# Kernel optimization log

Hardware: AMD Instinct MI355X
Metric: run time of the kernel (lower is better)

The kernel has to match this reference:

```python
import jax, jax.numpy as jnp
import numpy as np
from jax import lax

B, HH, WW, C = 8, 128, 128, 192
FL = 3  # focal_level
HID = 4 * C

def _gelu(x):
    return jax.nn.gelu(x, approximate=False)

def _ln(x, g, b, eps=1e-5):
    m = jnp.mean(x, axis=-1, keepdims=True)
    v = jnp.mean(jnp.square(x - m), axis=-1, keepdims=True)
    return (x - m) * lax.rsqrt(v + eps) * g + b

def _dwconv(x, k):
    # x: (B,C,H,W), k: (C,kh,kw) depthwise kernel
    return lax.conv_general_dilated(x, k[:, None], (1, 1), 'SAME',
                                    feature_group_count=x.shape[1],
                                    dimension_numbers=('NCHW', 'OIHW', 'NCHW'))

def setup_inputs() -> dict:
    key = jax.random.key(0)
    ks = jax.random.split(key, 12)
    s = 0.02
    return {
        'x': jax.random.normal(ks[0], (B, HH * WW, C), jnp.float32),
        'ln1_g': jnp.ones((C,), jnp.float32),
        'ln1_b': jnp.zeros((C,), jnp.float32),
        'f_w': jax.random.normal(ks[1], (C, 2 * C + FL + 1), jnp.float32) * s,
        'f_b': jnp.zeros((2 * C + FL + 1,), jnp.float32),
        'fk0': jax.random.normal(ks[2], (C, 3, 3), jnp.float32) * s,
        'fk1': jax.random.normal(ks[3], (C, 5, 5), jnp.float32) * s,
        'fk2': jax.random.normal(ks[4], (C, 7, 7), jnp.float32) * s,
        'h_w': jax.random.normal(ks[5], (C, C), jnp.float32) * s,
        'h_b': jnp.zeros((C,), jnp.float32),
        'proj_w': jax.random.normal(ks[6], (C, C), jnp.float32) * s,
        'proj_b': jnp.zeros((C,), jnp.float32),
        'ln2_g': jnp.ones((C,), jnp.float32),
        'ln2_b': jnp.zeros((C,), jnp.float32),
        'fc1_w': jax.random.normal(ks[7], (C, HID), jnp.float32) * s,
        'fc1_b': jnp.zeros((HID,), jnp.float32),
        'fc2_w': jax.random.normal(ks[8], (HID, C), jnp.float32) * s,
        'fc2_b': jnp.zeros((C,), jnp.float32),
        'H': HH,
        'W': WW,
    }

def reference(x, ln1_g, ln1_b, f_w, f_b, fk0, fk1, fk2, h_w, h_b,
              proj_w, proj_b, ln2_g, ln2_b, fc1_w, fc1_b, fc2_w, fc2_b, H, W):
    b, L, c = x.shape
    shortcut = x
    t = _ln(x, ln1_g, ln1_b).reshape(b, H, W, c)
    # f projection: (B,H,W,2C+FL+1) -> (B, 2C+FL+1, H, W)
    f = (t @ f_w + f_b).transpose(0, 3, 1, 2)
    q, ctx, gates = f[:, :c], f[:, c:2 * c], f[:, 2 * c:]
    ctx_all = jnp.zeros_like(ctx)
    for l, k in enumerate((fk0, fk1, fk2)):
        ctx = _gelu(_dwconv(ctx, k))
        ctx_all = ctx_all + ctx * gates[:, l:l + 1]
    ctx_global = _gelu(jnp.mean(ctx, axis=(2, 3), keepdims=True))
    ctx_all = ctx_all + ctx_global * gates[:, FL:]
    # h: 1x1 conv over channels
    modulator = jnp.einsum('oc,bchw->bohw', h_w, ctx_all) + h_b[None, :, None, None]
    x_out = (q * modulator).transpose(0, 2, 3, 1)  # (B,H,W,C)
    x_out = (x_out @ proj_w + proj_b).reshape(b, L, c)
    x1 = shortcut + x_out
    y = _ln(x1, ln2_g, ln2_b)
    y = _gelu(y @ fc1_w + fc1_b) @ fc2_w + fc2_b
    return x1 + y
```

## Files before the change

### kernel.cpp

```cpp
#include <hip/hip_runtime.h>
#include <hip/hip_bf16.h>

#define BB   8
#define HGT  128
#define WID  128
#define CC   192
#define LLEN (HGT*WID)
#define MM   (BB*LLEN)
#define NF   388
#define HIDN 768

typedef unsigned short us16;
typedef __attribute__((ext_vector_type(8))) short bf16x8;
typedef __attribute__((ext_vector_type(4))) float f32x4;

__device__ __forceinline__ float bf2f(us16 u) {
    return __uint_as_float(((unsigned int)u) << 16);
}
__device__ __forceinline__ us16 f2bf(float f) {
    unsigned int x = __float_as_uint(f);
    x = (x + 0x7fffu + ((x >> 16) & 1u)) >> 16;
    return (us16)x;
}
__device__ __forceinline__ float gelu_f(float x) {
    float u = 0.7978845608f * x * (1.0f + 0.044715f * x * x);
    float e = __expf(fminf(2.0f * u, 30.0f));
    return 0.5f * x * (1.0f + (e - 1.0f) / (e + 1.0f));
}

__device__ __forceinline__ void gload_lds16(const void* g, void* l) {
    __builtin_amdgcn_global_load_lds(
        (const __attribute__((address_space(1))) void*)g,
        (__attribute__((address_space(3))) void*)l, 16, 0, 0);
}

__global__ __launch_bounds__(256) void wcvt_kernel(const float* __restrict__ f_w,
        const float* __restrict__ h_w, const float* __restrict__ proj_w,
        const float* __restrict__ fc1_w, const float* __restrict__ fc2_w,
        const float* __restrict__ fk0, const float* __restrict__ fk1,
        const float* __restrict__ fk2,
        us16* __restrict__ fwT, us16* __restrict__ hwB, us16* __restrict__ projT,
        us16* __restrict__ w1T, us16* __restrict__ w2T,
        us16* __restrict__ kw0T, us16* __restrict__ kw1T, us16* __restrict__ kw2T) {
    int i = blockIdx.x * 256 + threadIdx.x;
    if (i < 86016) {
        int n = i / 192, k = i % 192;
        fwT[i] = (n < NF) ? f2bf(f_w[k * NF + n]) : (us16)0;
        return;
    }
    i -= 86016;
    if (i < 36864) { hwB[i] = f2bf(h_w[i]); return; }
    i -= 36864;
    if (i < 36864) { int n = i / 192, k = i % 192; projT[i] = f2bf(proj_w[k * CC + n]); return; }
    i -= 36864;
    if (i < 147456) { int n = i / 192, k = i % 192; w1T[i] = f2bf(fc1_w[k * HIDN + n]); return; }
    i -= 147456;
    if (i < 147456) { int n = i / 768, k = i % 768; w2T[i] = f2bf(fc2_w[k * CC + n]); return; }
    i -= 147456;
    if (i < 1728)  { int kyx = i / 192, c = i % 192; kw0T[i] = f2bf(fk0[c * 9 + kyx]);  return; }
    i -= 1728;
    if (i < 4800)  { int kyx = i / 192, c = i % 192; kw1T[i] = f2bf(fk1[c * 25 + kyx]); return; }
    i -= 4800;
    if (i < 9408)  { int kyx = i / 192, c = i % 192; kw2T[i] = f2bf(fk2[c * 49 + kyx]); return; }
}

__global__ __launch_bounds__(256) void ln_kernel(const float* __restrict__ in,
                                                 const float* __restrict__ g,
                                                 const float* __restrict__ b,
                                                 us16* __restrict__ out) {
    int wid  = threadIdx.x >> 6;
    int lane = threadIdx.x & 63;
    int row  = blockIdx.x * 4 + wid;
    const float* p = in + (size_t)row * CC;
    float v0 = p[lane], v1 = p[lane + 64], v2 = p[lane + 128];
    float s1 = v0 + v1 + v2;
    float s2 = v0*v0 + v1*v1 + v2*v2;
    for (int o = 32; o; o >>= 1) { s1 += __shfl_xor(s1, o); s2 += __shfl_xor(s2, o); }
    float m   = s1 * (1.0f / 192.0f);
    float var = s2 * (1.0f / 192.0f) - m * m;
    float inv = rsqrtf(var + 1e-5f);
    us16* q = out + (size_t)row * CC;
    q[lane]       = f2bf((v0 - m) * inv * g[lane]       + b[lane]);
    q[lane + 64]  = f2bf((v1 - m) * inv * g[lane + 64]  + b[lane + 64]);
    q[lane + 128] = f2bf((v2 - m) * inv * g[lane + 128] + b[lane + 128]);
}

template<int MODE>
__global__ __launch_bounds__(256) void mgemm_kernel(const us16* __restrict__ A,
        const us16* __restrict__ Bt, const float* __restrict__ bias,
        us16* __restrict__ out_q, us16* __restrict__ out_ctx, us16* __restrict__ out_g,
        const us16* __restrict__ q_in, const us16* __restrict__ gates_in,
        const float* __restrict__ hg, const float* __restrict__ x_in,
        float* __restrict__ out_f) {
    __shared__ __align__(16) char Asm[128 * 384];
    constexpr int NT = (MODE == 0) ? 7 : 3;
    int id  = blockIdx.x;
    int xcd = id & 7;
    int s   = id >> 3;
    int mt  = xcd * 128 + s / NT;
    int nt  = s % NT;
    int m0 = mt * 128, n0 = nt * 64;
    int tid = threadIdx.x, lane = tid & 63, w = tid >> 6;
    int wm = w >> 1, wn = w & 1, g = lane >> 4, lr = lane & 15;

    const char* Agl = (const char*)(A + (size_t)m0 * CC);
    #pragma unroll
    for (int i = 0; i < 12; i++) {
        int wl   = w * 12 + i;
        int byte = wl * 1024 + lane * 16;
        int row  = byte / 384;
        int off  = byte - row * 384;
        int soff = off ^ ((row & 7) << 4);
        gload_lds16(Agl + (size_t)row * 384 + soff, Asm + wl * 1024);
    }
    const us16* Bb = Bt + (size_t)(n0 + wn * 32 + lr) * CC;
    bf16x8 bfr[6][2];
    #pragma unroll
    for (int kk = 0; kk < 6; kk++)
        #pragma unroll
        for (int j = 0; j < 2; j++)
            bfr[kk][j] = *(const bf16x8*)(Bb + (size_t)j * 16 * CC + kk * 32 + g * 8);

    __syncthreads();

    f32x4 acc[4][2] = {};
    #pragma unroll
    for (int kk = 0; kk < 6; kk++) {
        int k2 = (kk * 32 + g * 8) * 2;
        bf16x8 a[4];
        #pragma unroll
        for (int i = 0; i < 4; i++) {
            int row = wm * 64 + i * 16 + lr;
            a[i] = *(const bf16x8*)(Asm + row * 384 + (k2 ^ ((row & 7) << 4)));
        }
        #pragma unroll
        for (int j = 0; j < 2; j++) {
            acc[0][j] = __builtin_amdgcn_mfma_f32_16x16x32_bf16(a[0], bfr[kk][j], acc[0][j], 0, 0, 0);
            acc[1][j] = __builtin_amdgcn_mfma_f32_16x16x32_bf16(a[1], bfr[kk][j], acc[1][j], 0, 0, 0);
            acc[2][j] = __builtin_amdgcn_mfma_f32_16x16x32_bf16(a[2], bfr[kk][j], acc[2][j], 0, 0, 0);
            acc[3][j] = __builtin_amdgcn_mfma_f32_16x16x32_bf16(a[3], bfr[kk][j], acc[3][j], 0, 0, 0);
        }
    }
    int orow = m0 + wm * 64;
    #pragma unroll
    for (int i = 0; i < 4; i++) {
        #pragma unroll
        for (int j = 0; j < 2; j++) {
            int ncol = n0 + wn * 32 + j * 16;
            int cc   = ncol + lr;
            #pragma unroll
            for (int r = 0; r < 4; r++) {
                int row = orow + i * 16 + g * 4 + r;
                float v = acc[i][j][r];
                if (MODE == 0) {
                    if (ncol < 192)      out_q[(size_t)row * CC + cc]          = f2bf(v + bias[cc]);
                    else if (ncol < 384) out_ctx[(size_t)row * CC + (cc - 192)] = f2bf(v + bias[cc]);
                    else if (cc < NF)    out_g[(size_t)row * 4 + (cc - 384)]    = f2bf(v + bias[cc]);
                } else if (MODE == 1) {
                    int bidx = row >> 14;
                    float val = v + bias[cc] + bf2f(gates_in[(size_t)row * 4 + 3]) * hg[bidx * CC + cc];
                    val *= bf2f(q_in[(size_t)row * CC + cc]);
                    out_q[(size_t)row * CC + cc] = f2bf(val);
                } else {
                    out_f[(size_t)row * CC + cc] = v + bias[cc] + x_in[(size_t)row * CC + cc];
                }
            }
        }
    }
}

template<int F, int LVL>
__global__ __launch_bounds__(256) void convv2_kernel(const us16* __restrict__ in,
                            us16* __restrict__ outp,
                            us16* __restrict__ ctx,
                            const us16* __restrict__ gates,
                            const us16* __restrict__ kwT,
                            float* __restrict__ partial) {
    constexpr int P  = F / 2;
    constexpr int NW = F + 3;
    __shared__ __align__(16) us16 kws[F * F * CC];
    __shared__ float psum[256][8];
    int tid = threadIdx.x;
    int lb  = (blockIdx.x & 7) * 384 + (blockIdx.x >> 3);
    for (int t = tid; t < F * F * CC / 8; t += 256)
        ((bf16x8*)kws)[t] = ((const bf16x8*)kwT)[t];
    __syncthreads();
    int idx  = lb * 256 + tid;
    int cg   = idx % 24;
    int rest = idx / 24;
    int x4 = rest & 31;
    int y0 = (rest >> 5) & 127;
    int b  = rest >> 12;
    int x0 = x4 * 4;
    float acc[4][8] = {};
    const us16* inb = in + (size_t)b * LLEN * CC + cg * 8;
    for (int ky = 0; ky < F; ky++) {
        int yy = y0 + ky - P;
        if (yy < 0 || yy > 127) continue;
        const us16* rp = inb + (size_t)yy * WID * CC;
        float rv[NW][8];
        #pragma unroll
        for (int i = 0; i < NW; i++) {
            int xx = x0 - P + i;
            if (xx >= 0 && xx <= 127) {
                bf16x8 v = *(const bf16x8*)(rp + (size_t)xx * CC);
                #pragma unroll
                for (int j = 0; j < 8; j++) rv[i][j] = bf2f((us16)v[j]);
            } else {
                #pragma unroll
                for (int j = 0; j < 8; j++) rv[i][j] = 0.0f;
            }
        }
        #pragma unroll
        for (int kx = 0; kx < F; kx++) {
            bf16x8 wv = *(const bf16x8*)(kws + (ky * F + kx) * CC + cg * 8);
            float w[8];
            #pragma unroll
            for (int j = 0; j < 8; j++) w[j] = bf2f((us16)wv[j]);
            #pragma unroll
            for (int px = 0; px < 4; px++)
                #pragma unroll
                for (int j = 0; j < 8; j++)
                    acc[px][j] += rv[kx + px][j] * w[j];
        }
    }
    int pix = (b * HGT + y0) * WID + x0;
    size_t obase = (size_t)pix * CC + cg * 8;
    if constexpr (LVL == 0) {
        #pragma unroll
        for (int px = 0; px < 4; px++) {
            bf16x8 ov;
            #pragma unroll
            for (int j = 0; j < 8; j++) ov[j] = (short)f2bf(gelu_f(acc[px][j]));
            *(bf16x8*)(outp + obase + (size_t)px * CC) = ov;
        }
    } else if constexpr (LVL == 1) {
        #pragma unroll
        for (int px = 0; px < 4; px++) {
            unsigned gv = *(const unsigned*)(gates + (size_t)(pix + px) * 4);
            float g0 = bf2f((us16)(gv & 0xffffu));
            float g1 = bf2f((us16)(gv >> 16));
            bf16x8 c3v = *(const bf16x8*)(inb + ((size_t)y0 * WID + x0 + px) * CC);
            bf16x8 ov, cv;
            #pragma unroll
            for (int j = 0; j < 8; j++) {
                float v5 = gelu_f(acc[px][j]);
                ov[j] = (short)f2bf(v5);
                cv[j] = (short)f2bf(g0 * bf2f((us16)c3v[j]) + g1 * v5);
            }
            *(bf16x8*)(outp + obase + (size_t)px * CC) = ov;
            *(bf16x8*)(ctx  + obase + (size_t)px * CC) = cv;
        }
    } else {
        float csum[8] = {};
        #pragma unroll
        for (int px = 0; px < 4; px++) {
            float g2 = bf2f(gates[(size_t)(pix + px) * 4 + 2]);
            bf16x8 cv = *(const bf16x8*)(ctx + obase + (size_t)px * CC);
            bf16x8 ov;
            #pragma unroll
            for (int j = 0; j < 8; j++) {
                float c7 = gelu_f(acc[px][j]);
                csum[j] += c7;
                ov[j] = (short)f2bf(bf2f((us16)cv[j]) + g2 * c7);
            }
            *(bf16x8*)(ctx + obase + (size_t)px * CC) = ov;
        }
        #pragma unroll
        for (int j = 0; j < 8; j++) psum[tid][j] = csum[j];
        __syncthreads();
        if (tid < 192) {
            int j = tid & 7, cgw = tid >> 3;
            int t0 = (cgw - (lb * 256) % 24) % 24;
            if (t0 < 0) t0 += 24;
            float s = 0.0f;
            for (int t = t0; t < 256; t += 24) s += psum[t][j];
            partial[(size_t)lb * CC + tid] = s;
        }
    }
}

__global__ __launch_bounds__(192) void gmean2_kernel(const float* __restrict__ partial,
                                                     const float* __restrict__ h_w,
                                                     float* __restrict__ hg) {
    __shared__ float ctxg[CC];
    int b = blockIdx.x, c = threadIdx.x;
    const float* pb = partial + (size_t)b * 384 * CC + c;
    float s = 0.0f;
    for (int k = 0; k < 384; k++) s += pb[(size_t)k * CC];
    ctxg[c] = gelu_f(s * (1.0f / 16384.0f));
    __syncthreads();
    float a = 0.0f;
    for (int c2 = 0; c2 < CC; c2++) a += h_w[c * CC + c2] * ctxg[c2];
    hg[b * CC + c] = a;
}

__global__ __launch_bounds__(512, 4) void fc1_kernel(const us16* __restrict__ A,
        const us16* __restrict__ w1T, const float* __restrict__ bias,
        us16* __restrict__ hid0, us16* __restrict__ hid1) {
    __shared__ __align__(16) char Asm[128 * 384];
    int id  = blockIdx.x;
    int swz = (id & 7) * 384 + (id >> 3);
    int mt  = swz / 6, nt = swz % 6;
    int m0 = mt * 128;
    int n0 = nt * 128;
    int tid = threadIdx.x, lane = tid & 63, w = tid >> 6;
    int wm = w >> 2, wn = w & 3, g = lane >> 4, lr = lane & 15;

    const char* Agl = (const char*)(A + (size_t)m0 * CC);
    #pragma unroll
    for (int i = 0; i < 6; i++) {
        int wl   = w * 6 + i;
        int byte = wl * 1024 + lane * 16;
        int row  = byte / 384;
        int off  = byte - row * 384;
        int soff = off ^ ((row & 7) << 4);
        gload_lds16(Agl + (size_t)row * 384 + soff, Asm + wl * 1024);
    }
    const us16* Bb = w1T + (size_t)(n0 + wn * 32 + lr) * CC;
    bf16x8 bfr[6][2];
    #pragma unroll
    for (int kk = 0; kk < 6; kk++)
        #pragma unroll
        for (int j = 0; j < 2; j++)
            bfr[kk][j] = *(const bf16x8*)(Bb + (size_t)j * 16 * CC + kk * 32 + g * 8);

    __syncthreads();

    f32x4 acc[4][2] = {};
    #pragma unroll
    for (int kk = 0; kk < 6; kk++) {
        int k2 = (kk * 32 + g * 8) * 2;
        bf16x8 a[4];
        #pragma unroll
        for (int i = 0; i < 4; i++) {
            int row = wm * 64 + i * 16 + lr;
            a[i] = *(const bf16x8*)(Asm + row * 384 + (k2 ^ ((row & 7) << 4)));
        }
        #pragma unroll
        for (int j = 0; j < 2; j++) {
            acc[0][j] = __builtin_amdgcn_mfma_f32_16x16x32_bf16(a[0], bfr[kk][j], acc[0][j], 0, 0, 0);
            acc[1][j] = __builtin_amdgcn_mfma_f32_16x16x32_bf16(a[1], bfr[kk][j], acc[1][j], 0, 0, 0);
            acc[2][j] = __builtin_amdgcn_mfma_f32_16x16x32_bf16(a[2], bfr[kk][j], acc[2][j], 0, 0, 0);
            acc[3][j] = __builtin_amdgcn_mfma_f32_16x16x32_bf16(a[3], bfr[kk][j], acc[3][j], 0, 0, 0);
        }
    }
    us16* hidp = (m0 & 32768) ? hid1 : hid0;
    int ml = (m0 & 32767) + wm * 64;
    #pragma unroll
    for (int i = 0; i < 4; i++) {
        #pragma unroll
        for (int j = 0; j < 2; j++) {
            int col = n0 + wn * 32 + j * 16 + lr;
            float fb = bias[col];
            #pragma unroll
            for (int r = 0; r < 4; r++) {
                int row = ml + i * 16 + g * 4 + r;
                hidp[(size_t)row * HIDN + col] = f2bf(gelu_f(acc[i][j][r] + fb));
            }
        }
    }
}

__global__ __launch_bounds__(512, 4) void fc2_kernel(const us16* __restrict__ hid0,
        const us16* __restrict__ hid1, const us16* __restrict__ w2T,
        const float* __restrict__ bias, float* __restrict__ io) {
    __shared__ __align__(16) char Asm[128 * 384];
    int m0 = blockIdx.x * 128;
    int tid = threadIdx.x, lane = tid & 63, w = tid >> 6;
    int wm = w >> 2, wn = w & 3, g = lane >> 4, lr = lane & 15;
    const us16* hidp = (m0 & 32768) ? hid1 : hid0;
    const char* Agl = (const char*)(hidp + (size_t)(m0 & 32767) * HIDN);

    f32x4 acc[4][3] = {};
    for (int c = 0; c < 4; c++) {
        #pragma unroll
        for (int i = 0; i < 6; i++) {
            int wl   = w * 6 + i;
            int byte = wl * 1024 + lane * 16;
            int row  = byte / 384;
            int off  = byte - row * 384;
            int soff = off ^ ((row & 7) << 4);
            gload_lds16(Agl + (size_t)row * 1536 + c * 384 + soff, Asm + wl * 1024);
        }
        __syncthreads();
        #pragma unroll
        for (int kk = 0; kk < 6; kk++) {
            int k2 = (kk * 32 + g * 8) * 2;
            bf16x8 a[4];
            #pragma unroll
            for (int i = 0; i < 4; i++) {
                int row = wm * 64 + i * 16 + lr;
                a[i] = *(const bf16x8*)(Asm + row * 384 + (k2 ^ ((row & 7) << 4)));
            }
            #pragma unroll
            for (int j = 0; j < 3; j++) {
                bf16x8 bv = *(const bf16x8*)(w2T + (size_t)(wn * 48 + j * 16 + lr) * HIDN
                                             + c * 192 + kk * 32 + g * 8);
                acc[0][j] = __builtin_amdgcn_mfma_f32_16x16x32_bf16(a[0], bv, acc[0][j], 0, 0, 0);
                acc[1][j] = __builtin_amdgcn_mfma_f32_16x16x32_bf16(a[1], bv, acc[1][j], 0, 0, 0);
                acc[2][j] = __builtin_amdgcn_mfma_f32_16x16x32_bf16(a[2], bv, acc[2][j], 0, 0, 0);
                acc[3][j] = __builtin_amdgcn_mfma_f32_16x16x32_bf16(a[3], bv, acc[3][j], 0, 0, 0);
            }
        }
        __syncthreads();
    }
    #pragma unroll
    for (int i = 0; i < 4; i++) {
        #pragma unroll
        for (int j = 0; j < 3; j++) {
            int col = wn * 48 + j * 16 + lr;
            float fb = bias[col];
            #pragma unroll
            for (int r = 0; r < 4; r++) {
                int row = m0 + wm * 64 + i * 16 + g * 4 + r;
                io[(size_t)row * CC + col] += acc[i][j][r] + fb;
            }
        }
    }
}

extern "C" void kernel_launch(void* const* d_in, const int* in_sizes, int n_in,
                              void* d_out, int out_size, void* d_ws, size_t ws_size,
                              hipStream_t stream) {
    const float* x      = (const float*)d_in[0];
    const float* ln1_g  = (const float*)d_in[1];
    const float* ln1_b  = (const float*)d_in[2];
    const float* f_w    = (const float*)d_in[3];
    const float* f_b    = (const float*)d_in[4];
    const float* fk0    = (const float*)d_in[5];
    const float* fk1    = (const float*)d_in[6];
    const float* fk2    = (const float*)d_in[7];
    const float* h_w    = (const float*)d_in[8];
    const float* h_b    = (const float*)d_in[9];
    const float* proj_w = (const float*)d_in[10];
    const float* proj_b = (const float*)d_in[11];
    const float* ln2_g  = (const float*)d_in[12];
    const float* ln2_b  = (const float*)d_in[13];
    const float* fc1_w  = (const float*)d_in[14];
    const float* fc1_b  = (const float*)d_in[15];
    const float* fc2_w  = (const float*)d_in[16];
    const float* fc2_b  = (const float*)d_in[17];
    float* outp = (float*)d_out;

    char* ws = (char*)d_ws;
    const size_t S = (size_t)MM * CC * 2;
    us16* t_buf   = (us16*)(ws);
    us16* q_buf   = (us16*)(ws + S);
    us16* ctx_all = (us16*)(ws + 2 * S);
    us16* gates   = (us16*)(ws + 3 * S);
    float* hg      = (float*)(ws + 3 * S + 1048576);
    us16* fwT   = (us16*)(ws + 3 * S + 1048576 + 786432 + 6144);
    us16* hwB   = fwT + 86016;
    us16* projT = hwB + 36864;
    us16* w1T   = projT + 36864;
    us16* w2T   = w1T + 147456;
    us16* kw0T  = w2T + 147456;
    us16* kw1T  = kw0T + 1728;
    us16* kw2T  = kw1T + 4800;
    us16* ctxA = (us16*)d_out;
    us16* ctxB = (us16*)d_out + (size_t)MM * CC;
    float* partial = (float*)ctxB;

    wcvt_kernel<<<1839, 256, 0, stream>>>(f_w, h_w, proj_w, fc1_w, fc2_w,
                                          fk0, fk1, fk2,
                                          fwT, hwB, projT, w1T, w2T, kw0T, kw1T, kw2T);

    ln_kernel<<<MM / 4, 256, 0, stream>>>(x, ln1_g, ln1_b, t_buf);

    mgemm_kernel<0><<<8 * 128 * 7, 256, 0, stream>>>(
        t_buf, fwT, f_b, q_buf, ctxA, gates, nullptr, nullptr, nullptr, nullptr, nullptr);

    convv2_kernel<3, 0><<<3072, 256, 0, stream>>>(ctxA, ctxB, nullptr, nullptr, kw0T, nullptr);
    convv2_kernel<5, 1><<<3072, 256, 0, stream>>>(ctxB, ctxA, ctx_all, gates, kw1T, nullptr);
    convv2_kernel<7, 2><<<3072, 256, 0, stream>>>(ctxA, nullptr, ctx_all, gates, kw2T, partial);

    gmean2_kernel<<<8, 192, 0, stream>>>(partial, h_w, hg);

    mgemm_kernel<1><<<8 * 128 * 3, 256, 0, stream>>>(
        ctx_all, hwB, h_b, t_buf, nullptr, nullptr, q_buf, gates, hg, nullptr, nullptr);

    mgemm_kernel<2><<<8 * 128 * 3, 256, 0, stream>>>(
        t_buf, projT, proj_b, nullptr, nullptr, nullptr, nullptr, nullptr, nullptr, x, outp);

    ln_kernel<<<MM / 4, 256, 0, stream>>>(outp, ln2_g, ln2_b, q_buf);

    for (int h = 0; h < 2; h++) {
        const us16* Ah = q_buf + (size_t)h * 65536 * CC;
        float* ioh     = outp  + (size_t)h * 65536 * CC;
        fc1_kernel<<<3072, 512, 0, stream>>>(Ah, w1T, fc1_b, t_buf, ctx_all);
        fc2_kernel<<<512, 512, 0, stream>>>(t_buf, ctx_all, w2T, fc2_b, ioh);
    }
}
```

Measured before the change: 738.9 us.

## Fuse layernorms into following GEMMs and merge modulator with projection

LayerNorm1 is computed directly into shared memory inside the f-projection GEMM, which now loops over all seven N tiles per block. The h-projection, modulation and output projection are merged into one kernel that keeps the modulated tile in LDS. LayerNorm2 is fused into fc1, with each block covering all six N tiles. The conv kernel reuses its weight LDS for partial sums. Together these remove several intermediate global round-trips and kernel launches, at the cost of fewer blocks, more serial work per block and larger register footprints.

Measured after the change: 933.9 us. +26.4%, slower.

```diff
diff --git a/kernel.cpp b/kernel.cpp
--- a/kernel.cpp
+++ b/kernel.cpp
@@ -64,105 +64,71 @@
     if (i < 9408)  { int kyx = i / 192, c = i % 192; kw2T[i] = f2bf(fk2[c * 49 + kyx]); return; }
 }
 
-__global__ __launch_bounds__(256) void ln_kernel(const float* __restrict__ in,
-                                                 const float* __restrict__ g,
-                                                 const float* __restrict__ b,
-                                                 us16* __restrict__ out) {
-    int wid  = threadIdx.x >> 6;
-    int lane = threadIdx.x & 63;
-    int row  = blockIdx.x * 4 + wid;
-    const float* p = in + (size_t)row * CC;
-    float v0 = p[lane], v1 = p[lane + 64], v2 = p[lane + 128];
-    float s1 = v0 + v1 + v2;
-    float s2 = v0*v0 + v1*v1 + v2*v2;
-    for (int o = 32; o; o >>= 1) { s1 += __shfl_xor(s1, o); s2 += __shfl_xor(s2, o); }
-    float m   = s1 * (1.0f / 192.0f);
-    float var = s2 * (1.0f / 192.0f) - m * m;
-    float inv = rsqrtf(var + 1e-5f);
-    us16* q = out + (size_t)row * CC;
-    q[lane]       = f2bf((v0 - m) * inv * g[lane]       + b[lane]);
-    q[lane + 64]  = f2bf((v1 - m) * inv * g[lane + 64]  + b[lane + 64]);
-    q[lane + 128] = f2bf((v2 - m) * inv * g[lane + 128] + b[lane + 128]);
-}
-
-template<int MODE>
-__global__ __launch_bounds__(256) void mgemm_kernel(const us16* __restrict__ A,
-        const us16* __restrict__ Bt, const float* __restrict__ bias,
-        us16* __restrict__ out_q, us16* __restrict__ out_ctx, us16* __restrict__ out_g,
-        const us16* __restrict__ q_in, const us16* __restrict__ gates_in,
-        const float* __restrict__ hg, const float* __restrict__ x_in,
-        float* __restrict__ out_f) {
+__global__ __launch_bounds__(256) void lngemm_kernel(const float* __restrict__ x,
+        const float* __restrict__ lg, const float* __restrict__ lb,
+        const us16* __restrict__ fwT, const float* __restrict__ bias,
+        us16* __restrict__ out_q, us16* __restrict__ out_ctx, us16* __restrict__ out_g) {
     __shared__ __align__(16) char Asm[128 * 384];
-    constexpr int NT = (MODE == 0) ? 7 : 3;
-    int id  = blockIdx.x;
-    int xcd = id & 7;
-    int s   = id >> 3;
-    int mt  = xcd * 128 + s / NT;
-    int nt  = s % NT;
-    int m0 = mt * 128, n0 = nt * 64;
+    int id = blockIdx.x;
+    int mt = (id & 7) * 128 + (id >> 3);
+    int m0 = mt * 128;
     int tid = threadIdx.x, lane = tid & 63, w = tid >> 6;
-    int wm = w >> 1, wn = w & 1, g = lane >> 4, lr = lane & 15;
-
-    const char* Agl = (const char*)(A + (size_t)m0 * CC);
-    #pragma unroll
-    for (int i = 0; i < 12; i++) {
-        int wl   = w * 12 + i;
-        int byte = wl * 1024 + lane * 16;
-        int row  = byte / 384;
-        int off  = byte - row * 384;
-        int soff = off ^ ((row & 7) << 4);
-        gload_lds16(Agl + (size_t)row * 384 + soff, Asm + wl * 1024);
-    }
-    const us16* Bb = Bt + (size_t)(n0 + wn * 32 + lr) * CC;
-    bf16x8 bfr[6][2];
-    #pragma unroll
-    for (int kk = 0; kk < 6; kk++)
-        #pragma unroll
-        for (int j = 0; j < 2; j++)
-            bfr[kk][j] = *(const bf16x8*)(Bb + (size_t)j * 16 * CC + kk * 32 + g * 8);
-
+    int wm = w >> 1, wn = w & 1, g4 = lane >> 4, lr = lane & 15;
+    float gg0 = lg[lane], gg1 = lg[lane + 64], gg2 = lg[lane + 128];
+    float bb0 = lb[lane], bb1 = lb[lane + 64], bb2 = lb[lane + 128];
+    for (int rr = 0; rr < 32; rr++) {
+        int rb = w * 32 + rr;
+        const float* p = x + (size_t)(m0 + rb) * CC;
+        float v0 = p[lane], v1 = p[lane + 64], v2 = p[lane + 128];
+        float s1 = v0 + v1 + v2, s2 = v0*v0 + v1*v1 + v2*v2;
+        for (int o = 32; o; o >>= 1) { s1 += __shfl_xor(s1, o); s2 += __shfl_xor(s2, o); }
+        float m = s1 * (1.0f / 192.0f);
+        float inv = rsqrtf(s2 * (1.0f / 192.0f) - m * m + 1e-5f);
+        int sw = (rb & 7) << 4;
+        *(us16*)(Asm + ((rb * 384 + lane * 2)         ^ sw)) = f2bf((v0 - m) * inv * gg0 + bb0);
+        *(us16*)(Asm + ((rb * 384 + (lane + 64) * 2)  ^ sw)) = f2bf((v1 - m) * inv * gg1 + bb1);
+        *(us16*)(Asm + ((rb * 384 + (lane + 128) * 2) ^ sw)) = f2bf((v2 - m) * inv * gg2 + bb2);
+    }
     __syncthreads();
-
-    f32x4 acc[4][2] = {};
+    bf16x8 af[6][4];
     #pragma unroll
     for (int kk = 0; kk < 6; kk++) {
-        int k2 = (kk * 32 + g * 8) * 2;
-        bf16x8 a[4];
+        int k2 = (kk * 32 + g4 * 8) * 2;
         #pragma unroll
         for (int i = 0; i < 4; i++) {
             int row = wm * 64 + i * 16 + lr;
-            a[i] = *(const bf16x8*)(Asm + row * 384 + (k2 ^ ((row & 7) << 4)));
-        }
-        #pragma unroll
-        for (int j = 0; j < 2; j++) {
-            acc[0][j] = __builtin_amdgcn_mfma_f32_16x16x32_bf16(a[0], bfr[kk][j], acc[0][j], 0, 0, 0);
-            acc[1][j] = __builtin_amdgcn_mfma_f32_16x16x32_bf16(a[1], bfr[kk][j], acc[1][j], 0, 0, 0);
-            acc[2][j] = __builtin_amdgcn_mfma_f32_16x16x32_bf16(a[2], bfr[kk][j], acc[2][j], 0, 0, 0);
-            acc[3][j] = __builtin_amdgcn_mfma_f32_16x16x32_bf16(a[3], bfr[kk][j], acc[3][j], 0, 0, 0);
+            af[kk][i] = *(const bf16x8*)(Asm + row * 384 + (k2 ^ ((row & 7) << 4)));
         }
     }
     int orow = m0 + wm * 64;
     #pragma unroll
-    for (int i = 0; i < 4; i++) {
-        #pragma unroll
-        for (int j = 0; j < 2; j++) {
-            int ncol = n0 + wn * 32 + j * 16;
-            int cc   = ncol + lr;
-            #pragma unroll
-            for (int r = 0; r < 4; r++) {
-                int row = orow + i * 16 + g * 4 + r;
-                float v = acc[i][j][r];
-                if (MODE == 0) {
-                    if (ncol < 192)      out_q[(size_t)row * CC + cc]          = f2bf(v + bias[cc]);
-                    else if (ncol < 384) out_ctx[(size_t)row * CC + (cc - 192)] = f2bf(v + bias[cc]);
-                    else if (cc < NF)    out_g[(size_t)row * 4 + (cc - 384)]    = f2bf(v + bias[cc]);
-                } else if (MODE == 1) {
-                    int bidx = row >> 14;
-                    float val = v + bias[cc] + bf2f(gates_in[(size_t)row * 4 + 3]) * hg[bidx * CC + cc];
-                    val *= bf2f(q_in[(size_t)row * CC + cc]);
-                    out_q[(size_t)row * CC + cc] = f2bf(val);
-                } else {
-                    out_f[(size_t)row * CC + cc] = v + bias[cc] + x_in[(size_t)row * CC + cc];
+    for (int nt = 0; nt < 7; nt++) {
+        int n0 = nt * 64;
+        const us16* Bb = fwT + (size_t)(n0 + wn * 32 + lr) * CC;
+        f32x4 acc[4][2] = {};
+        #pragma unroll
+        for (int kk = 0; kk < 6; kk++) {
+            #pragma unroll
+            for (int j = 0; j < 2; j++) {
+                bf16x8 bv = *(const bf16x8*)(Bb + (size_t)j * 16 * CC + kk * 32 + g4 * 8);
+                #pragma unroll
+                for (int i = 0; i < 4; i++)
+                    acc[i][j] = __builtin_amdgcn_mfma_f32_16x16x32_bf16(af[kk][i], bv, acc[i][j], 0, 0, 0);
+            }
+        }
+        #pragma unroll
+        for (int i = 0; i < 4; i++) {
+            #pragma unroll
+            for (int j = 0; j < 2; j++) {
+                int ncol = n0 + wn * 32 + j * 16;
+                int cc   = ncol + lr;
+                #pragma unroll
+                for (int r = 0; r < 4; r++) {
+                    int row = orow + i * 16 + g4 * 4 + r;
+                    float v = acc[i][j][r];
+                    if (ncol < 192)      out_q[(size_t)row * CC + cc]            = f2bf(v + bias[cc]);
+                    else if (ncol < 384) out_ctx[(size_t)row * CC + (cc - 192)]  = f2bf(v + bias[cc]);
+                    else if (cc < NF)    out_g[(size_t)row * 4 + (cc - 384)]     = f2bf(v + bias[cc]);
                 }
             }
         }
@@ -179,7 +145,6 @@
     constexpr int P  = F / 2;
     constexpr int NW = F + 3;
     __shared__ __align__(16) us16 kws[F * F * CC];
-    __shared__ float psum[256][8];
     int tid = threadIdx.x;
     int lb  = (blockIdx.x & 7) * 384 + (blockIdx.x >> 3);
     for (int t = tid; t < F * F * CC / 8; t += 256)
@@ -266,6 +231,8 @@
             }
             *(bf16x8*)(ctx + obase + (size_t)px * CC) = ov;
         }
+        __syncthreads();
+        float (*psum)[8] = (float (*)[8])kws;
         #pragma unroll
         for (int j = 0; j < 8; j++) psum[tid][j] = csum[j];
         __syncthreads();
@@ -295,68 +262,165 @@
     hg[b * CC + c] = a;
 }
 
-__global__ __launch_bounds__(512, 4) void fc1_kernel(const us16* __restrict__ A,
-        const us16* __restrict__ w1T, const float* __restrict__ bias,
-        us16* __restrict__ hid0, us16* __restrict__ hid1) {
+__global__ __launch_bounds__(256) void modproj_kernel(const us16* __restrict__ A,
+        const us16* __restrict__ hwB, const float* __restrict__ h_b,
+        const us16* __restrict__ projT, const float* __restrict__ proj_b,
+        const us16* __restrict__ q_in, const us16* __restrict__ gates_in,
+        const float* __restrict__ hg, const float* __restrict__ x_in,
+        float* __restrict__ out_f) {
     __shared__ __align__(16) char Asm[128 * 384];
-    int id  = blockIdx.x;
-    int swz = (id & 7) * 384 + (id >> 3);
-    int mt  = swz / 6, nt = swz % 6;
+    int id = blockIdx.x;
+    int mt = (id & 7) * 128 + (id >> 3);
     int m0 = mt * 128;
-    int n0 = nt * 128;
     int tid = threadIdx.x, lane = tid & 63, w = tid >> 6;
-    int wm = w >> 2, wn = w & 3, g = lane >> 4, lr = lane & 15;
+    int wm = w >> 1, wn = w & 1, g4 = lane >> 4, lr = lane & 15;
 
     const char* Agl = (const char*)(A + (size_t)m0 * CC);
     #pragma unroll
-    for (int i = 0; i < 6; i++) {
-        int wl   = w * 6 + i;
+    for (int i = 0; i < 12; i++) {
+        int wl   = w * 12 + i;
         int byte = wl * 1024 + lane * 16;
         int row  = byte / 384;
         int off  = byte - row * 384;
         int soff = off ^ ((row & 7) << 4);
         gload_lds16(Agl + (size_t)row * 384 + soff, Asm + wl * 1024);
     }
-    const us16* Bb = w1T + (size_t)(n0 + wn * 32 + lr) * CC;
-    bf16x8 bfr[6][2];
-    #pragma unroll
-    for (int kk = 0; kk < 6; kk++)
-        #pragma unroll
-        for (int j = 0; j < 2; j++)
-            bfr[kk][j] = *(const bf16x8*)(Bb + (size_t)j * 16 * CC + kk * 32 + g * 8);
-
     __syncthreads();
-
-    f32x4 acc[4][2] = {};
-    #pragma unroll
-    for (int kk = 0; kk < 6; kk++) {
-        int k2 = (kk * 32 + g * 8) * 2;
-        bf16x8 a[4];
+    {
+        f32x4 acc[4][6] = {};
+        #pragma unroll
+        for (int kk = 0; kk < 6; kk++) {
+            int k2 = (kk * 32 + g4 * 8) * 2;
+            bf16x8 a[4];
+            #pragma unroll
+            for (int i = 0; i < 4; i++) {
+                int row = wm * 64 + i * 16 + lr;
+                a[i] = *(const bf16x8*)(Asm + row * 384 + (k2 ^ ((row & 7) << 4)));
+            }
+            #pragma unroll
+            for (int j = 0; j < 6; j++) {
+                bf16x8 bv = *(const bf16x8*)(hwB + (size_t)(wn * 96 + j * 16 + lr) * CC + kk * 32 + g4 * 8);
+                #pragma unroll
+                for (int i = 0; i < 4; i++)
+                    acc[i][j] = __builtin_amdgcn_mfma_f32_16x16x32_bf16(a[i], bv, acc[i][j], 0, 0, 0);
+            }
+        }
+        __syncthreads();
+        int bidx = m0 >> 14;
         #pragma unroll
         for (int i = 0; i < 4; i++) {
-            int row = wm * 64 + i * 16 + lr;
-            a[i] = *(const bf16x8*)(Asm + row * 384 + (k2 ^ ((row & 7) << 4)));
-        }
-        #pragma unroll
-        for (int j = 0; j < 2; j++) {
-            acc[0][j] = __builtin_amdgcn_mfma_f32_16x16x32_bf16(a[0], bfr[kk][j], acc[0][j], 0, 0, 0);
-            acc[1][j] = __builtin_amdgcn_mfma_f32_16x16x32_bf16(a[1], bfr[kk][j], acc[1][j], 0, 0, 0);
-            acc[2][j] = __builtin_amdgcn_mfma_f32_16x16x32_bf16(a[2], bfr[kk][j], acc[2][j], 0, 0, 0);
-            acc[3][j] = __builtin_amdgcn_mfma_f32_16x16x32_bf16(a[3], bfr[kk][j], acc[3][j], 0, 0, 0);
-        }
-    }
+            #pragma unroll
+            for (int r = 0; r < 4; r++) {
+                int rl  = wm * 64 + i * 16 + g4 * 4 + r;
+                int row = m0 + rl;
+                float g3 = bf2f(gates_in[(size_t)row * 4 + 3]);
+                int sw = (rl & 7) << 4;
+                #pragma unroll
+                for (int j = 0; j < 6; j++) {
+                    int cc = wn * 96 + j * 16 + lr;
+                    float val = (acc[i][j][r] + h_b[cc] + g3 * hg[bidx * CC + cc])
+                                * bf2f(q_in[(size_t)row * CC + cc]);
+                    *(us16*)(Asm + ((rl * 384 + cc * 2) ^ sw)) = f2bf(val);
+                }
+            }
+        }
+    }
+    __syncthreads();
+    {
+        f32x4 acc[4][6] = {};
+        #pragma unroll
+        for (int kk = 0; kk < 6; kk++) {
+            int k2 = (kk * 32 + g4 * 8) * 2;
+            bf16x8 a[4];
+            #pragma unroll
+            for (int i = 0; i < 4; i++) {
+                int row = wm * 64 + i * 16 + lr;
+                a[i] = *(const bf16x8*)(Asm + row * 384 + (k2 ^ ((row & 7) << 4)));
+            }
+            #pragma unroll
+            for (int j = 0; j < 6; j++) {
+                bf16x8 bv = *(const bf16x8*)(projT + (size_t)(wn * 96 + j * 16 + lr) * CC + kk * 32 + g4 * 8);
+                #pragma unroll
+                for (int i = 0; i < 4; i++)
+                    acc[i][j] = __builtin_amdgcn_mfma_f32_16x16x32_bf16(a[i], bv, acc[i][j], 0, 0, 0);
+            }
+        }
+        #pragma unroll
+        for (int i = 0; i < 4; i++) {
+            #pragma unroll
+            for (int j = 0; j < 6; j++) {
+                int cc = wn * 96 + j * 16 + lr;
+                float pb = proj_b[cc];
+                #pragma unroll
+                for (int r = 0; r < 4; r++) {
+                    int row = m0 + wm * 64 + i * 16 + g4 * 4 + r;
+                    out_f[(size_t)row * CC + cc] = acc[i][j][r] + pb + x_in[(size_t)row * CC + cc];
+                }
+            }
+        }
+    }
+}
+
+__global__ __launch_bounds__(512) void fc1ln_kernel(const float* __restrict__ x1,
+        const float* __restrict__ lg, const float* __restrict__ lb,
+        const us16* __restrict__ w1T, const float* __restrict__ bias,
+        us16* __restrict__ hid0, us16* __restrict__ hid1) {
+    __shared__ __align__(16) char Asm[128 * 384];
+    int id  = blockIdx.x;
+    int swz = (id & 7) * 64 + (id >> 3);
+    int m0  = swz * 128;
+    int tid = threadIdx.x, lane = tid & 63, w = tid >> 6;
+    int wm = w >> 2, wn = w & 3, g4 = lane >> 4, lr = lane & 15;
+    float gg0 = lg[lane], gg1 = lg[lane + 64], gg2 = lg[lane + 128];
+    float bb0 = lb[lane], bb1 = lb[lane + 64], bb2 = lb[lane + 128];
+    for (int rr = 0; rr < 16; rr++) {
+        int rb = w * 16 + rr;
+        const float* p = x1 + (size_t)(m0 + rb) * CC;
+        float v0 = p[lane], v1 = p[lane + 64], v2 = p[lane + 128];
+        float s1 = v0 + v1 + v2, s2 = v0*v0 + v1*v1 + v2*v2;
+        for (int o = 32; o; o >>= 1) { s1 += __shfl_xor(s1, o); s2 += __shfl_xor(s2, o); }
+        float m = s1 * (1.0f / 192.0f);
+        float inv = rsqrtf(s2 * (1.0f / 192.0f) - m * m + 1e-5f);
+        int sw = (rb & 7) << 4;
+        *(us16*)(Asm + ((rb * 384 + lane * 2)         ^ sw)) = f2bf((v0 - m) * inv * gg0 + bb0);
+        *(us16*)(Asm + ((rb * 384 + (lane + 64) * 2)  ^ sw)) = f2bf((v1 - m) * inv * gg1 + bb1);
+        *(us16*)(Asm + ((rb * 384 + (lane + 128) * 2) ^ sw)) = f2bf((v2 - m) * inv * gg2 + bb2);
+    }
+    __syncthreads();
     us16* hidp = (m0 & 32768) ? hid1 : hid0;
     int ml = (m0 & 32767) + wm * 64;
-    #pragma unroll
-    for (int i = 0; i < 4; i++) {
-        #pragma unroll
-        for (int j = 0; j < 2; j++) {
-            int col = n0 + wn * 32 + j * 16 + lr;
-            float fb = bias[col];
-            #pragma unroll
-            for (int r = 0; r < 4; r++) {
-                int row = ml + i * 16 + g * 4 + r;
-                hidp[(size_t)row * HIDN + col] = f2bf(gelu_f(acc[i][j][r] + fb));
+    for (int nt = 0; nt < 6; nt++) {
+        int n0 = nt * 128;
+        const us16* Bb = w1T + (size_t)(n0 + wn * 32 + lr) * CC;
+        f32x4 acc[4][2] = {};
+        #pragma unroll
+        for (int kk = 0; kk < 6; kk++) {
+            int k2 = (kk * 32 + g4 * 8) * 2;
+            bf16x8 a[4];
+            #pragma unroll
+            for (int i = 0; i < 4; i++) {
+                int row = wm * 64 + i * 16 + lr;
+                a[i] = *(const bf16x8*)(Asm + row * 384 + (k2 ^ ((row & 7) << 4)));
+            }
+            #pragma unroll
+            for (int j = 0; j < 2; j++) {
+                bf16x8 bv = *(const bf16x8*)(Bb + (size_t)j * 16 * CC + kk * 32 + g4 * 8);
+                #pragma unroll
+                for (int i = 0; i < 4; i++)
+                    acc[i][j] = __builtin_amdgcn_mfma_f32_16x16x32_bf16(a[i], bv, acc[i][j], 0, 0, 0);
+            }
+        }
+        #pragma unroll
+        for (int i = 0; i < 4; i++) {
+            #pragma unroll
+            for (int j = 0; j < 2; j++) {
+                int col = n0 + wn * 32 + j * 16 + lr;
+                float fb = bias[col];
+                #pragma unroll
+                for (int r = 0; r < 4; r++) {
+                    int row = ml + i * 16 + g4 * 4 + r;
+                    hidp[(size_t)row * HIDN + col] = f2bf(gelu_f(acc[i][j][r] + fb));
+                }
             }
         }
     }
@@ -466,10 +530,8 @@
                                           fk0, fk1, fk2,
                                           fwT, hwB, projT, w1T, w2T, kw0T, kw1T, kw2T);
 
-    ln_kernel<<<MM / 4, 256, 0, stream>>>(x, ln1_g, ln1_b, t_buf);
-
-    mgemm_kernel<0><<<8 * 128 * 7, 256, 0, stream>>>(
-        t_buf, fwT, f_b, q_buf, ctxA, gates, nullptr, nullptr, nullptr, nullptr, nullptr);
+    lngemm_kernel<<<1024, 256, 0, stream>>>(x, ln1_g, ln1_b, fwT, f_b,
+                                            q_buf, ctxA, gates);
 
     convv2_kernel<3, 0><<<3072, 256, 0, stream>>>(ctxA, ctxB, nullptr, nullptr, kw0T, nullptr);
     convv2_kernel<5, 1><<<3072, 256, 0, stream>>>(ctxB, ctxA, ctx_all, gates, kw1T, nullptr);
@@ -477,18 +539,14 @@
 
     gmean2_kernel<<<8, 192, 0, stream>>>(partial, h_w, hg);
 
-    mgemm_kernel<1><<<8 * 128 * 3, 256, 0, stream>>>(
-        ctx_all, hwB, h_b, t_buf, nullptr, nullptr, q_buf, gates, hg, nullptr, nullptr);
-
-    mgemm_kernel<2><<<8 * 128 * 3, 256, 0, stream>>>(
-        t_buf, projT, proj_b, nullptr, nullptr, nullptr, nullptr, nullptr, nullptr, x, outp);
-
-    ln_kernel<<<MM / 4, 256, 0, stream>>>(outp, ln2_g, ln2_b, q_buf);
+    modproj_kernel<<<1024, 256, 0, stream>>>(ctx_all, hwB, h_b, projT, proj_b,
+                                             q_buf, gates, hg, x, outp);
 
     for (int h = 0; h < 2; h++) {
-        const us16* Ah = q_buf + (size_t)h * 65536 * CC;
-        float* ioh     = outp  + (size_t)h * 65536 * CC;
-        fc1_kernel<<<3072, 512, 0, stream>>>(Ah, w1T, fc1_b, t_buf, ctx_all);
-        fc2_kernel<<<512, 512, 0, stream>>>(t_buf, ctx_all, w2T, fc2_b, ioh);
-    }
-}
+        const float* x1h = outp + (size_t)h * 65536 * CC;
+        fc1ln_kernel<<<512, 512, 0, stream>>>(x1h, ln2_g, ln2_b, w1T, fc1_b,
+                                              t_buf, ctx_all);
+        fc2_kernel<<<512, 512, 0, stream>>>(t_buf, ctx_all, w2T, fc2_b,
+                                            (float*)x1h);
+    }
+}
```
